# Kernel tuning notes

Measured on AMD Instinct MI355X. Metric: run time of the kernel, lower is better.

Reference implementation:

```python
import jax, jax.numpy as jnp
import numpy as np

B, C, H, W = 8, 384, 32, 32
NH = 6
HD = C // NH          # 64
T = H * W             # 1024
EPS = 1e-5            # torch InstanceNorm2d default


def setup_inputs() -> dict:
    key = jax.random.key(0)
    ks = jax.random.split(key, 8)
    s = 1.0 / np.sqrt(C)  # keep pre-softmax logits in a sane range
    x = jax.random.normal(ks[0], (B, C, H, W), dtype=jnp.float32)
    Wq = jax.random.normal(ks[1], (C, C), dtype=jnp.float32) * s
    Wk = jax.random.normal(ks[2], (C, C), dtype=jnp.float32) * s
    Wv = jax.random.normal(ks[3], (C, C), dtype=jnp.float32) * s
    head_w = jax.random.normal(ks[4], (NH, NH), dtype=jnp.float32) * (1.0 / np.sqrt(NH))
    gamma = jnp.ones((NH,), dtype=jnp.float32)
    beta = jnp.zeros((NH,), dtype=jnp.float32)
    projW = jax.random.normal(ks[5], (C, C), dtype=jnp.float32) * s
    projb = jnp.zeros((C,), dtype=jnp.float32)
    return {"x": x, "Wq": Wq, "Wk": Wk, "Wv": Wv, "head_w": head_w,
            "gamma": gamma, "beta": beta, "projW": projW, "projb": projb}


def reference(x, Wq, Wk, Wv, head_w, gamma, beta, projW, projb):
    b, c, h, w = x.shape
    t = h * w
    scale = HD ** (-0.5)
    xf = x.reshape(b, c, t)                               # [B,C,T]
    # 1x1 convs == channel GEMMs; conv weight [Cout,Cin]
    q = jnp.einsum('oc,bct->bot', Wq, xf).reshape(b, NH, HD, t)
    k = jnp.einsum('oc,bct->bot', Wk, xf).reshape(b, NH, HD, t)
    v = jnp.einsum('oc,bct->bot', Wv, xf).reshape(b, NH, HD, t)
    # raw scores [B,h,T,T], scaled
    scores = jnp.einsum('bhdq,bhdt->bhqt', q, k) * scale
    # cross-head 1x1 conv mix: out-head g from in-head h
    mixed = jnp.einsum('gh,bhqt->bgqt', head_w, scores)
    attn = jax.nn.softmax(mixed, axis=-1)
    # InstanceNorm2d over spatial dims (q,T) per (b,head), biased variance
    mean = jnp.mean(attn, axis=(2, 3), keepdims=True)
    var = jnp.var(attn, axis=(2, 3), keepdims=True)
    attn = (attn - mean) * jax.lax.rsqrt(var + EPS)
    attn = attn * gamma[None, :, None, None] + beta[None, :, None, None]
    # value matmul: v is [B,h,d,T]
    out = jnp.einsum('bhqt,bhdt->bhqd', attn, v)          # [B,h,T,d]
    # faithful row-major reshape (matches torch .view(B, T, C))
    out = out.reshape(b, t, c)
    y = out @ projW.T + projb                              # Linear(C,C)
    return jnp.transpose(y, (0, 2, 1)).reshape(b, c, h, w)
```

## Files before the change

kernel.cpp:

```cpp
#include <hip/hip_runtime.h>
#include <hip/hip_bf16.h>
#include <cstdint>

typedef __bf16 bf16_t;
typedef __bf16 bf16x8 __attribute__((ext_vector_type(8)));
typedef float  f32x4  __attribute__((ext_vector_type(4)));

#define MFMA16(a, b, c) __builtin_amdgcn_mfma_f32_16x16x32_bf16((a), (b), (c), 0, 0, 0)

constexpr int BB = 8, CC = 384, NHH = 6, TT = 1024;

union U8 { uint4 u; bf16_t h[8]; };
union U2 { unsigned int u; bf16_t h[2]; };

struct CastArgs {
    const void* src[9];
    bf16_t*     dst[9];
    int         n[9];
};

__global__ __launch_bounds__(256) void cast_kernel(CastArgs a)
{
    const bool isbf = (((const unsigned short*)a.src[5])[0] == 0x3F80u);
    const int ai = blockIdx.y;
    const int n  = a.n[ai];
    bf16_t* dst  = a.dst[ai];
    const int t0     = (blockIdx.x * 256 + threadIdx.x) * 8;
    const int stride = gridDim.x * 256 * 8;
    if (isbf) {
        const bf16_t* s = (const bf16_t*)a.src[ai];
        for (int idx = t0; idx < n; idx += stride) {
            if (idx + 8 <= n) *(uint4*)(dst + idx) = *(const uint4*)(s + idx);
            else for (int j = 0; idx + j < n; ++j) dst[idx + j] = s[idx + j];
        }
    } else {
        const float* s = (const float*)a.src[ai];
        for (int idx = t0; idx < n; idx += stride) {
            if (idx + 8 <= n) {
                f32x4 v0 = *(const f32x4*)(s + idx);
                f32x4 v1 = *(const f32x4*)(s + idx + 4);
                U8 o;
                #pragma unroll
                for (int j = 0; j < 4; ++j) { o.h[j] = (bf16_t)v0[j]; o.h[4 + j] = (bf16_t)v1[j]; }
                *(uint4*)(dst + idx) = o.u;
            } else for (int j = 0; idx + j < n; ++j) dst[idx + j] = (bf16_t)s[idx + j];
        }
    }
}

__global__ __launch_bounds__(256) void qkv_kernel(
    const bf16_t* __restrict__ x,
    const bf16_t* __restrict__ Wq,
    const bf16_t* __restrict__ Wk,
    const bf16_t* __restrict__ Wv,
    const bf16_t* __restrict__ head_w,
    bf16_t* __restrict__ Qmix,
    bf16_t* __restrict__ kT,
    bf16_t* __restrict__ vm)
{
    const int og = blockIdx.x;
    const int tt = blockIdx.y;
    const int b  = blockIdx.z;
    const int t0 = tt * 64;
    const int tid  = threadIdx.x;
    const int lane = tid & 63;
    const int wid  = tid >> 6;
    const int quad = lane >> 4;
    const int l16  = lane & 15;

    __shared__ __align__(16) bf16_t xT[64][CC + 8];
    __shared__ float smixL[36];

    if (tid < 36) smixL[tid] = 0.125f * (float)head_w[tid];
    {
        const bf16_t* xb = x + (size_t)b * CC * TT;
        const int tq = tid & 7;
        const int cp = tid >> 3;
        #pragma unroll
        for (int pass = 0; pass < 6; ++pass) {
            const int c = (pass * 32 + cp) * 2;
            U8 r0, r1;
            r0.u = *(const uint4*)(xb + (size_t)c * TT + t0 + tq * 8);
            r1.u = *(const uint4*)(xb + (size_t)(c + 1) * TT + t0 + tq * 8);
            #pragma unroll
            for (int j = 0; j < 8; ++j) {
                U2 p; p.h[0] = r0.h[j]; p.h[1] = r1.h[j];
                *(unsigned int*)&xT[tq * 8 + j][c] = p.u;
            }
        }
    }
    __syncthreads();

    const bf16_t* W = (og < 2) ? Wq : (og < 4) ? Wk : Wv;
    const int obase = (og & 1) * 192 + wid * 48;

    if (og < 4) {
        f32x4 acc[3][4];
        const f32x4 zero = {0.f, 0.f, 0.f, 0.f};
        #pragma unroll
        for (int mi = 0; mi < 3; ++mi)
            #pragma unroll
            for (int ni = 0; ni < 4; ++ni) acc[mi][ni] = zero;

        for (int k0 = 0; k0 < CC; k0 += 32) {
            bf16x8 afr[3];
            #pragma unroll
            for (int mi = 0; mi < 3; ++mi)
                afr[mi] = *(const bf16x8*)(W + (size_t)(obase + mi * 16 + l16) * CC + k0 + quad * 8);
            #pragma unroll
            for (int ni = 0; ni < 4; ++ni) {
                bf16x8 bfr = *(const bf16x8*)&xT[ni * 16 + l16][k0 + quad * 8];
                #pragma unroll
                for (int mi = 0; mi < 3; ++mi)
                    acc[mi][ni] = MFMA16(afr[mi], bfr, acc[mi][ni]);
            }
        }

        if (og < 2) {
            for (int g = 0; g < 6; ++g) {
                bf16_t* dst = Qmix + (size_t)(b * NHH + g) * TT * CC;
                #pragma unroll
                for (int mi = 0; mi < 3; ++mi)
                    #pragma unroll
                    for (int ni = 0; ni < 4; ++ni) {
                        const int o0 = obase + mi * 16 + quad * 4;
                        const int tl = t0 + ni * 16 + l16;
                        const float m = smixL[g * 6 + (o0 >> 6)];
                        U2 lo2, hi2;
                        lo2.h[0] = (bf16_t)(acc[mi][ni][0] * m); lo2.h[1] = (bf16_t)(acc[mi][ni][1] * m);
                        hi2.h[0] = (bf16_t)(acc[mi][ni][2] * m); hi2.h[1] = (bf16_t)(acc[mi][ni][3] * m);
                        uint2 pk; pk.x = lo2.u; pk.y = hi2.u;
                        *(uint2*)(dst + (size_t)tl * CC + o0) = pk;
                    }
            }
        } else {
            #pragma unroll
            for (int mi = 0; mi < 3; ++mi)
                #pragma unroll
                for (int ni = 0; ni < 4; ++ni) {
                    const int o0 = obase + mi * 16 + quad * 4;
                    const int tl = t0 + ni * 16 + l16;
                    U2 lo2, hi2;
                    lo2.h[0] = (bf16_t)acc[mi][ni][0]; lo2.h[1] = (bf16_t)acc[mi][ni][1];
                    hi2.h[0] = (bf16_t)acc[mi][ni][2]; hi2.h[1] = (bf16_t)acc[mi][ni][3];
                    uint2 pk; pk.x = lo2.u; pk.y = hi2.u;
                    *(uint2*)(kT + ((size_t)b * TT + tl) * CC + o0) = pk;
                }
        }
    } else {
        f32x4 acc[4][3];
        const f32x4 zero = {0.f, 0.f, 0.f, 0.f};
        #pragma unroll
        for (int mi = 0; mi < 4; ++mi)
            #pragma unroll
            for (int ni = 0; ni < 3; ++ni) acc[mi][ni] = zero;

        for (int k0 = 0; k0 < CC; k0 += 32) {
            bf16x8 bfr[3];
            #pragma unroll
            for (int ni = 0; ni < 3; ++ni)
                bfr[ni] = *(const bf16x8*)(W + (size_t)(obase + ni * 16 + l16) * CC + k0 + quad * 8);
            #pragma unroll
            for (int mi = 0; mi < 4; ++mi) {
                bf16x8 afr = *(const bf16x8*)&xT[mi * 16 + l16][k0 + quad * 8];
                #pragma unroll
                for (int ni = 0; ni < 3; ++ni)
                    acc[mi][ni] = MFMA16(afr, bfr[ni], acc[mi][ni]);
            }
        }

        #pragma unroll
        for (int mi = 0; mi < 4; ++mi)
            #pragma unroll
            for (int ni = 0; ni < 3; ++ni) {
                const int ol  = obase + ni * 16 + l16;
                const int tl0 = mi * 16 + quad * 4;
                U2 lo2, hi2;
                lo2.h[0] = (bf16_t)acc[mi][ni][0]; lo2.h[1] = (bf16_t)acc[mi][ni][1];
                hi2.h[0] = (bf16_t)acc[mi][ni][2]; hi2.h[1] = (bf16_t)acc[mi][ni][3];
                uint2 pk; pk.x = lo2.u; pk.y = hi2.u;
                *(uint2*)(vm + ((size_t)b * CC + ol) * TT + t0 + tl0) = pk;
            }
    }
}

__global__ __launch_bounds__(256) void vrow_kernel(const bf16_t* __restrict__ vm,
                                                   float* __restrict__ vrs)
{
    const int bg = blockIdx.x;
    const int d  = threadIdx.x & 63;
    const int qr = threadIdx.x >> 6;
    const bf16_t* row = vm + ((size_t)(bg / 6) * CC + (bg % 6) * 64 + d) * TT + qr * 256;
    float s = 0.f;
    for (int i = 0; i < 256; i += 8) {
        U8 v; v.u = *(const uint4*)(row + i);
        #pragma unroll
        for (int j = 0; j < 8; ++j) s += (float)v.h[j];
    }
    __shared__ float red[4][64];
    red[qr][d] = s;
    __syncthreads();
    if (qr == 0) vrs[bg * 64 + d] = red[0][d] + red[1][d] + red[2][d] + red[3][d];
}

__global__ __launch_bounds__(256, 3) void fused_attn(
    const bf16_t* __restrict__ Qmix,
    const bf16_t* __restrict__ kT,
    const bf16_t* __restrict__ vm,
    float* __restrict__ Uhat,
    float* __restrict__ sumsq)
{
    const int L  = blockIdx.x;
    const int b  = L & 7;
    const int rr = L >> 3;
    const int qt = rr & 15;
    const int g  = rr >> 4;
    const int qbase = qt * 64;
    const int tid = threadIdx.x, lane = tid & 63, wid = tid >> 6;
    const int quad = lane >> 4, l16 = lane & 15;
    const int Msub = (wid & 1) * 64;
    const int Nsub = (wid >> 1) * 32;

    __shared__ __align__(16) bf16_t sm[12288];
    bf16_t* At = sm;
    bf16_t* Bt = sm + 8192;
    bf16_t* Ps = sm;
    bf16_t* Vt = sm + 4096;
    __shared__ float lred[4][2][16], l2red[4][2][16];
    __shared__ float lrowS[64];

    const bf16_t* kTb = kT + (size_t)b * TT * CC;
    const bf16_t* Qb  = Qmix + ((size_t)(b * NHH + g) * TT + qbase) * CC;
    const bf16_t* Vb  = vm + ((size_t)b * CC + g * 64) * TT;

    float lacc[2] = {0.f, 0.f}, l2acc[2] = {0.f, 0.f};
    f32x4 U[4];
    const f32x4 zero = {0.f, 0.f, 0.f, 0.f};
    #pragma unroll
    for (int n2 = 0; n2 < 4; ++n2) U[n2] = zero;

    for (int tt = 0; tt < 8; ++tt) {
        f32x4 S[4][2];
        #pragma unroll
        for (int mi = 0; mi < 4; ++mi)
            #pragma unroll
            for (int ni = 0; ni < 2; ++ni) S[mi][ni] = zero;

        for (int kk = 0; kk < 6; ++kk) {
            __syncthreads();
            #pragma unroll
            for (int it = 0; it < 4; ++it) {
                const int id = it * 256 + tid;
                const int row = id >> 3, ch = id & 7;
                U8 v; v.u = *(const uint4*)(kTb + (size_t)(tt * 128 + row) * CC + kk * 64 + ch * 8);
                *(uint4*)&At[row * 64 + ((ch ^ (row & 7)) * 8)] = v.u;
            }
            #pragma unroll
            for (int it = 0; it < 2; ++it) {
                const int id = it * 256 + tid;
                const int row = id >> 3, ch = id & 7;
                U8 v; v.u = *(const uint4*)(Qb + (size_t)row * CC + kk * 64 + ch * 8);
                *(uint4*)&Bt[row * 64 + ((ch ^ (row & 7)) * 8)] = v.u;
            }
            __syncthreads();
            #pragma unroll
            for (int k2 = 0; k2 < 2; ++k2) {
                const int sw = ((k2 * 4 + quad) ^ (l16 & 7)) * 8;
                bf16x8 a[4], bq[2];
                #pragma unroll
                for (int mi = 0; mi < 4; ++mi)
                    a[mi] = *(const bf16x8*)&At[(Msub + mi * 16 + l16) * 64 + sw];
                #pragma unroll
                for (int ni = 0; ni < 2; ++ni)
                    bq[ni] = *(const bf16x8*)&Bt[(Nsub + ni * 16 + l16) * 64 + sw];
                #pragma unroll
                for (int mi = 0; mi < 4; ++mi)
                    #pragma unroll
                    for (int ni = 0; ni < 2; ++ni)
                        S[mi][ni] = MFMA16(a[mi], bq[ni], S[mi][ni]);
            }
        }

        #pragma unroll
        for (int mi = 0; mi < 4; ++mi)
            #pragma unroll
            for (int ni = 0; ni < 2; ++ni)
                #pragma unroll
                for (int r = 0; r < 4; ++r) {
                    const float p = __expf(fminf(S[mi][ni][r], 60.0f));
                    S[mi][ni][r] = p;
                    lacc[ni]  += p;
                    l2acc[ni] += p * p;
                }

        __syncthreads();

        #pragma unroll
        for (int it = 0; it < 4; ++it) {
            const int id = it * 256 + tid;
            const int row = id >> 4, ch = id & 15;
            U8 v; v.u = *(const uint4*)(Vb + (size_t)row * TT + tt * 128 + ch * 8);
            *(uint4*)&Vt[row * 128 + ((((ch & 7) ^ (row & 7)) | (ch & 8)) * 8)] = v.u;
        }

        #pragma unroll
        for (int h = 0; h < 2; ++h) {
            if ((wid & 1) == h) {
                #pragma unroll
                for (int mi = 0; mi < 4; ++mi) {
                    const int tc = mi * 2 + (quad >> 1);
                    #pragma unroll
                    for (int ni = 0; ni < 2; ++ni) {
                        const int q = Nsub + ni * 16 + l16;
                        U2 lo2, hi2;
                        lo2.h[0] = (bf16_t)S[mi][ni][0]; lo2.h[1] = (bf16_t)S[mi][ni][1];
                        hi2.h[0] = (bf16_t)S[mi][ni][2]; hi2.h[1] = (bf16_t)S[mi][ni][3];
                        uint2 pk; pk.x = lo2.u; pk.y = hi2.u;
                        *(uint2*)&Ps[q * 64 + ((tc ^ (l16 & 7)) * 8) + (quad & 1) * 4] = pk;
                    }
                }
            }
            __syncthreads();
            bf16x8 ap[2];
            #pragma unroll
            for (int k2 = 0; k2 < 2; ++k2) {
                const int qa = wid * 16 + l16;
                ap[k2] = *(const bf16x8*)&Ps[qa * 64 + (((k2 * 4 + quad) ^ (l16 & 7)) * 8)];
            }
            #pragma unroll
            for (int n2 = 0; n2 < 4; ++n2) {
                const int d = n2 * 16 + l16;
                #pragma unroll
                for (int k2 = 0; k2 < 2; ++k2) {
                    const int tc = h * 8 + k2 * 4 + quad;
                    bf16x8 bv = *(const bf16x8*)&Vt[d * 128 + ((((tc & 7) ^ (l16 & 7)) | (tc & 8)) * 8)];
                    U[n2] = MFMA16(ap[k2], bv, U[n2]);
                }
            }
            __syncthreads();
        }
    }

    #pragma unroll
    for (int ni = 0; ni < 2; ++ni) {
        float l = lacc[ni], l2 = l2acc[ni];
        l  += __shfl_xor(l, 16, 64);  l  += __shfl_xor(l, 32, 64);
        l2 += __shfl_xor(l2, 16, 64); l2 += __shfl_xor(l2, 32, 64);
        if (quad == 0) { lred[wid][ni][l16] = l; l2red[wid][ni][l16] = l2; }
    }
    __syncthreads();
    if (tid < 64) {
        const int q = tid;
        const int w0 = (q >> 5) * 2, ni = (q >> 4) & 1, lo = q & 15;
        const float l  = lred[w0][ni][lo]  + lred[w0 + 1][ni][lo];
        const float l2 = l2red[w0][ni][lo] + l2red[w0 + 1][ni][lo];
        lrowS[q] = l;
        float c = l2 / (l * l);
        #pragma unroll
        for (int off = 1; off < 64; off <<= 1) c += __shfl_xor(c, off, 64);
        if (tid == 0) atomicAdd(&sumsq[b * NHH + g], c);
    }
    __syncthreads();

    float* Ub = Uhat + ((size_t)(b * NHH + g) * TT + qbase) * 64;
    #pragma unroll
    for (int r = 0; r < 4; ++r) {
        const int ql = wid * 16 + quad * 4 + r;
        const float invl = 1.0f / lrowS[ql];
        #pragma unroll
        for (int n2 = 0; n2 < 4; ++n2)
            Ub[(size_t)ql * 64 + n2 * 16 + l16] = U[n2][r] * invl;
    }
}

__global__ __launch_bounds__(256) void proj_kernel(
    const float* __restrict__ Uhat,
    const float* __restrict__ vrs,
    const float* __restrict__ sumsq,
    const bf16_t* __restrict__ gamma,
    const bf16_t* __restrict__ beta,
    const bf16_t* __restrict__ projW,
    const bf16_t* __restrict__ projb,
    float* __restrict__ out)
{
    const int ts = blockIdx.x;
    const int b  = blockIdx.y;
    const int t0 = ts * 32;
    const int tid = threadIdx.x, lane = tid & 63, wid = tid >> 6;
    const int quad = lane >> 4, l16 = lane & 15;

    __shared__ float Ac[6], Cc[6], pb[CC];
    if (tid < 6) {
        const float ss  = sumsq[b * NHH + tid];
        const float var = fmaxf(ss - 1.0f, 0.0f) * (1.0f / 1048576.0f);
        const float a   = (float)gamma[tid] * rsqrtf(var + 1e-5f);
        Ac[tid] = a;
        Cc[tid] = (float)beta[tid] - a * (1.0f / 1024.0f);
    }
    for (int i = tid; i < CC; i += 256) pb[i] = (float)projb[i];
    __syncthreads();

    f32x4 acc[6][2];
    const f32x4 zero = {0.f, 0.f, 0.f, 0.f};
    #pragma unroll
    for (int mi = 0; mi < 6; ++mi)
        #pragma unroll
        for (int ni = 0; ni < 2; ++ni) acc[mi][ni] = zero;

    const float* Ub = Uhat + (size_t)b * TT * CC;
    for (int k0 = 0; k0 < CC; k0 += 32) {
        bf16x8 bfr[2];
        #pragma unroll
        for (int ni = 0; ni < 2; ++ni) {
            const int tl = t0 + ni * 16 + l16;
            const int baseoff = tl * CC + k0 + quad * 8;
            f32x4 u0 = *(const f32x4*)(Ub + baseoff);
            f32x4 u1 = *(const f32x4*)(Ub + baseoff + 4);
            U8 z;
            #pragma unroll
            for (int j = 0; j < 8; ++j) {
                const int off = baseoff + j;
                const int h = off >> 16;
                const int d = off & 63;
                const float uv = (j < 4) ? u0[j] : u1[j - 4];
                z.h[j] = (bf16_t)(Ac[h] * uv + Cc[h] * vrs[(b * NHH + h) * 64 + d]);
            }
            bfr[ni] = *(const bf16x8*)&z;
        }
        #pragma unroll
        for (int mi = 0; mi < 6; ++mi) {
            const int o = wid * 96 + mi * 16 + l16;
            bf16x8 afr = *(const bf16x8*)(projW + (size_t)o * CC + k0 + quad * 8);
            #pragma unroll
            for (int ni = 0; ni < 2; ++ni)
                acc[mi][ni] = MFMA16(afr, bfr[ni], acc[mi][ni]);
        }
    }

    #pragma unroll
    for (int mi = 0; mi < 6; ++mi)
        #pragma unroll
        for (int ni = 0; ni < 2; ++ni)
            #pragma unroll
            for (int r = 0; r < 4; ++r) {
                const int o  = wid * 96 + mi * 16 + quad * 4 + r;
                const int tl = t0 + ni * 16 + l16;
                out[((size_t)b * CC + o) * TT + tl] = acc[mi][ni][r] + pb[o];
            }
}

extern "C" void kernel_launch(void* const* d_in, const int* in_sizes, int n_in,
                              void* d_out, int out_size, void* d_ws, size_t ws_size,
                              hipStream_t stream)
{
    float* outp = (float*)d_out;
    char* ws = (char*)d_ws;

    size_t off = 0;
    auto alloc = [&](size_t bytes) {
        void* p = ws + off;
        off += (bytes + 255) & ~(size_t)255;
        return p;
    };

    const size_t szQ = (size_t)BB * TT * CC * sizeof(bf16_t);

    bf16_t* cx  = (bf16_t*)alloc(szQ);
    bf16_t* cWq = (bf16_t*)alloc((size_t)CC * CC * 2);
    bf16_t* cWk = (bf16_t*)alloc((size_t)CC * CC * 2);
    bf16_t* cWv = (bf16_t*)alloc((size_t)CC * CC * 2);
    bf16_t* cPW = (bf16_t*)alloc((size_t)CC * CC * 2);
    bf16_t* chw = (bf16_t*)alloc(64 * 2);
    bf16_t* cg  = (bf16_t*)alloc(64 * 2);
    bf16_t* cb  = (bf16_t*)alloc(64 * 2);
    bf16_t* cpb = (bf16_t*)alloc(CC * 2);
    bf16_t* Qm  = (bf16_t*)alloc((size_t)BB * NHH * TT * CC * 2);
    bf16_t* kT  = (bf16_t*)alloc(szQ);
    bf16_t* vm  = (bf16_t*)alloc(szQ);
    float*  Uh  = (float*)alloc((size_t)BB * NHH * TT * 64 * 4);
    float*  vr  = (float*)alloc(48 * 64 * 4);
    float*  sq  = (float*)alloc(48 * 4);

    CastArgs ca;
    bf16_t* dsts[9] = {cx, cWq, cWk, cWv, chw, cg, cb, cPW, cpb};
    for (int i = 0; i < 9; ++i) {
        ca.src[i] = d_in[i];
        ca.dst[i] = dsts[i];
        ca.n[i]   = in_sizes[i];
    }

    hipMemsetAsync(sq, 0, 48 * sizeof(float), stream);
    cast_kernel<<<dim3(192, 9), 256, 0, stream>>>(ca);
    qkv_kernel<<<dim3(6, 16, 8), 256, 0, stream>>>(cx, cWq, cWk, cWv, chw, Qm, kT, vm);
    vrow_kernel<<<48, 256, 0, stream>>>(vm, vr);
    fused_attn<<<768, 256, 0, stream>>>(Qm, kT, vm, Uh, sq);
    proj_kernel<<<dim3(32, 8), 256, 0, stream>>>(Uh, vr, sq, cg, cb, cPW, cpb, outp);
}
```

Measured before the change: 219.0 us.

## Apply head mixing on score tiles in-kernel instead of materializing per-head mixed Q

Stops writing six head-mixed copies of Q. The attention kernel now computes raw per-head scores for all six heads at once, mixes them across heads in registers, and then takes the exponential. It splits the key range into two halves across blocks, with double-buffered K/V loads staged through registers. It also adds a stats kernel that merges the partial row sums and square sums and moves the 1/l normalization into the projection. This removes a large Q write and read and the repeated K reads per mixed head, at the cost of more registers, 512-thread blocks, and partial U buffers that the projection must sum.

```diff
diff --git a/kernel.cpp b/kernel.cpp
--- a/kernel.cpp
+++ b/kernel.cpp
@@ -53,8 +53,7 @@
     const bf16_t* __restrict__ Wq,
     const bf16_t* __restrict__ Wk,
     const bf16_t* __restrict__ Wv,
-    const bf16_t* __restrict__ head_w,
-    bf16_t* __restrict__ Qmix,
+    bf16_t* __restrict__ qT,
     bf16_t* __restrict__ kT,
     bf16_t* __restrict__ vm)
 {
@@ -69,9 +68,7 @@
     const int l16  = lane & 15;
 
     __shared__ __align__(16) bf16_t xT[64][CC + 8];
-    __shared__ float smixL[36];
-
-    if (tid < 36) smixL[tid] = 0.125f * (float)head_w[tid];
+
     {
         const bf16_t* xb = x + (size_t)b * CC * TT;
         const int tq = tid & 7;
@@ -116,37 +113,19 @@
             }
         }
 
-        if (og < 2) {
-            for (int g = 0; g < 6; ++g) {
-                bf16_t* dst = Qmix + (size_t)(b * NHH + g) * TT * CC;
-                #pragma unroll
-                for (int mi = 0; mi < 3; ++mi)
-                    #pragma unroll
-                    for (int ni = 0; ni < 4; ++ni) {
-                        const int o0 = obase + mi * 16 + quad * 4;
-                        const int tl = t0 + ni * 16 + l16;
-                        const float m = smixL[g * 6 + (o0 >> 6)];
-                        U2 lo2, hi2;
-                        lo2.h[0] = (bf16_t)(acc[mi][ni][0] * m); lo2.h[1] = (bf16_t)(acc[mi][ni][1] * m);
-                        hi2.h[0] = (bf16_t)(acc[mi][ni][2] * m); hi2.h[1] = (bf16_t)(acc[mi][ni][3] * m);
-                        uint2 pk; pk.x = lo2.u; pk.y = hi2.u;
-                        *(uint2*)(dst + (size_t)tl * CC + o0) = pk;
-                    }
-            }
-        } else {
-            #pragma unroll
-            for (int mi = 0; mi < 3; ++mi)
-                #pragma unroll
-                for (int ni = 0; ni < 4; ++ni) {
-                    const int o0 = obase + mi * 16 + quad * 4;
-                    const int tl = t0 + ni * 16 + l16;
-                    U2 lo2, hi2;
-                    lo2.h[0] = (bf16_t)acc[mi][ni][0]; lo2.h[1] = (bf16_t)acc[mi][ni][1];
-                    hi2.h[0] = (bf16_t)acc[mi][ni][2]; hi2.h[1] = (bf16_t)acc[mi][ni][3];
-                    uint2 pk; pk.x = lo2.u; pk.y = hi2.u;
-                    *(uint2*)(kT + ((size_t)b * TT + tl) * CC + o0) = pk;
-                }
-        }
+        bf16_t* dst = (og < 2) ? qT : kT;
+        #pragma unroll
+        for (int mi = 0; mi < 3; ++mi)
+            #pragma unroll
+            for (int ni = 0; ni < 4; ++ni) {
+                const int o0 = obase + mi * 16 + quad * 4;
+                const int tl = t0 + ni * 16 + l16;
+                U2 lo2, hi2;
+                lo2.h[0] = (bf16_t)acc[mi][ni][0]; lo2.h[1] = (bf16_t)acc[mi][ni][1];
+                hi2.h[0] = (bf16_t)acc[mi][ni][2]; hi2.h[1] = (bf16_t)acc[mi][ni][3];
+                uint2 pk; pk.x = lo2.u; pk.y = hi2.u;
+                *(uint2*)(dst + ((size_t)b * TT + tl) * CC + o0) = pk;
+            }
     } else {
         f32x4 acc[4][3];
         const f32x4 zero = {0.f, 0.f, 0.f, 0.f};
@@ -203,178 +182,219 @@
     if (qr == 0) vrs[bg * 64 + d] = red[0][d] + red[1][d] + red[2][d] + red[3][d];
 }
 
-__global__ __launch_bounds__(256, 3) void fused_attn(
-    const bf16_t* __restrict__ Qmix,
+__global__ __launch_bounds__(512, 2) void fused_attn(
+    const bf16_t* __restrict__ qT,
     const bf16_t* __restrict__ kT,
     const bf16_t* __restrict__ vm,
-    float* __restrict__ Uhat,
-    float* __restrict__ sumsq)
+    const bf16_t* __restrict__ head_w,
+    float* __restrict__ Up,
+    float* __restrict__ lp,
+    float* __restrict__ l2p)
 {
     const int L  = blockIdx.x;
     const int b  = L & 7;
     const int rr = L >> 3;
     const int qt = rr & 15;
-    const int g  = rr >> 4;
-    const int qbase = qt * 64;
+    const int th = rr >> 4;
+
     const int tid = threadIdx.x, lane = tid & 63, wid = tid >> 6;
     const int quad = lane >> 4, l16 = lane & 15;
-    const int Msub = (wid & 1) * 64;
-    const int Nsub = (wid >> 1) * 32;
-
-    __shared__ __align__(16) bf16_t sm[12288];
-    bf16_t* At = sm;
-    bf16_t* Bt = sm + 8192;
-    bf16_t* Ps = sm;
-    bf16_t* Vt = sm + 4096;
-    __shared__ float lred[4][2][16], l2red[4][2][16];
-    __shared__ float lrowS[64];
-
-    const bf16_t* kTb = kT + (size_t)b * TT * CC;
-    const bf16_t* Qb  = Qmix + ((size_t)(b * NHH + g) * TT + qbase) * CC;
-    const bf16_t* Vb  = vm + ((size_t)b * CC + g * 64) * TT;
-
-    float lacc[2] = {0.f, 0.f}, l2acc[2] = {0.f, 0.f};
-    f32x4 U[4];
+
+    __shared__ __align__(16) bf16_t sm[49152];
+    bf16_t* Ks = sm;
+    bf16_t* Ps = sm + 12288;
+    bf16_t* Vs = sm + 24576;
+    __shared__ float smix[36];
+
+    if (tid < 36) smix[tid] = 0.125f * (float)head_w[tid];
+
+    const int T0 = th * 512;
+
+    const int tsub = wid & 1;
+    const int sqh  = wid >> 1;
+    const int pqg  = wid >> 1;
+    const int pgg  = wid & 1;
+
+    bf16x8 qf[6][2];
+    {
+        const bf16_t* Qb = qT + ((size_t)b * TT + qt * 64 + sqh * 16 + l16) * CC + quad * 8;
+        #pragma unroll
+        for (int kk = 0; kk < 6; ++kk)
+            #pragma unroll
+            for (int k2 = 0; k2 < 2; ++k2)
+                qf[kk][k2] = *(const bf16x8*)(Qb + kk * 64 + k2 * 32);
+    }
+
+    const bf16_t* ksrc[3]; const bf16_t* vsrc[3];
+    int kdst[3], vdst[3];
+    #pragma unroll
+    for (int it = 0; it < 3; ++it) {
+        const int f  = it * 512 + tid;
+        const int kk = f >> 8, krow = (f >> 3) & 31, kch = f & 7;
+        ksrc[it] = kT + ((size_t)b * TT + T0 + krow) * CC + kk * 64 + (kch ^ (krow & 7)) * 8;
+        kdst[it] = f * 8;
+        const int vrow = f >> 2, vch = f & 3;
+        vsrc[it] = vm + ((size_t)b * CC + vrow) * TT + T0 + (vch ^ ((vrow >> 1) & 3)) * 8;
+        vdst[it] = f * 8;
+    }
+
+    uint4 kreg[3], vreg[3];
+    #pragma unroll
+    for (int it = 0; it < 3; ++it) {
+        kreg[it] = *(const uint4*)ksrc[it];
+        vreg[it] = *(const uint4*)vsrc[it];
+    }
+    __syncthreads();
+
+    float mixc[36];
+    #pragma unroll
+    for (int j = 0; j < 36; ++j)
+        mixc[j] = __uint_as_float(__builtin_amdgcn_readfirstlane(__float_as_uint(smix[j])));
+
+    #pragma unroll
+    for (int it = 0; it < 3; ++it) {
+        *(uint4*)&Ks[kdst[it]] = kreg[it];
+        *(uint4*)&Vs[vdst[it]] = vreg[it];
+        kreg[it] = *(const uint4*)(ksrc[it] + 32 * CC);
+        vreg[it] = *(const uint4*)(vsrc[it] + 32);
+    }
+    __syncthreads();
+
+    f32x4 Uacc[3][4];
     const f32x4 zero = {0.f, 0.f, 0.f, 0.f};
     #pragma unroll
-    for (int n2 = 0; n2 < 4; ++n2) U[n2] = zero;
-
-    for (int tt = 0; tt < 8; ++tt) {
-        f32x4 S[4][2];
-        #pragma unroll
-        for (int mi = 0; mi < 4; ++mi)
-            #pragma unroll
-            for (int ni = 0; ni < 2; ++ni) S[mi][ni] = zero;
-
+    for (int hh = 0; hh < 3; ++hh)
+        #pragma unroll
+        for (int n2 = 0; n2 < 4; ++n2) Uacc[hh][n2] = zero;
+    float lacc[6]  = {0.f, 0.f, 0.f, 0.f, 0.f, 0.f};
+    float l2acc[6] = {0.f, 0.f, 0.f, 0.f, 0.f, 0.f};
+
+    const int arow  = (tsub * 16 + l16) * 64;
+    const int aswz0 = ((quad)     ^ (l16 & 7)) * 8;
+    const int aswz1 = ((4 + quad) ^ (l16 & 7)) * 8;
+    const int prow  = (sqh * 16 + l16) * 32;
+    const int pswzW = ((tsub * 2 + (quad >> 1)) ^ ((l16 >> 1) & 3)) * 8 + (quad & 1) * 4;
+    const int parow = (pqg * 16 + l16) * 32;
+    const int pswzR = (quad ^ ((l16 >> 1) & 3)) * 8;
+
+    for (int t = 0; t < 16; ++t) {
+        f32x4 S[6];
+        #pragma unroll
         for (int kk = 0; kk < 6; ++kk) {
-            __syncthreads();
-            #pragma unroll
-            for (int it = 0; it < 4; ++it) {
-                const int id = it * 256 + tid;
-                const int row = id >> 3, ch = id & 7;
-                U8 v; v.u = *(const uint4*)(kTb + (size_t)(tt * 128 + row) * CC + kk * 64 + ch * 8);
-                *(uint4*)&At[row * 64 + ((ch ^ (row & 7)) * 8)] = v.u;
-            }
-            #pragma unroll
-            for (int it = 0; it < 2; ++it) {
-                const int id = it * 256 + tid;
-                const int row = id >> 3, ch = id & 7;
-                U8 v; v.u = *(const uint4*)(Qb + (size_t)row * CC + kk * 64 + ch * 8);
-                *(uint4*)&Bt[row * 64 + ((ch ^ (row & 7)) * 8)] = v.u;
-            }
-            __syncthreads();
-            #pragma unroll
-            for (int k2 = 0; k2 < 2; ++k2) {
-                const int sw = ((k2 * 4 + quad) ^ (l16 & 7)) * 8;
-                bf16x8 a[4], bq[2];
+            bf16x8 a0 = *(const bf16x8*)&Ks[kk * 2048 + arow + aswz0];
+            bf16x8 a1 = *(const bf16x8*)&Ks[kk * 2048 + arow + aswz1];
+            S[kk] = MFMA16(a0, qf[kk][0], zero);
+            S[kk] = MFMA16(a1, qf[kk][1], S[kk]);
+        }
+        uint2 pk[6];
+        #pragma unroll
+        for (int g = 0; g < 6; ++g) {
+            float mp[4];
+            #pragma unroll
+            for (int r = 0; r < 4; ++r) {
+                float m = mixc[g * 6] * S[0][r];
                 #pragma unroll
-                for (int mi = 0; mi < 4; ++mi)
-                    a[mi] = *(const bf16x8*)&At[(Msub + mi * 16 + l16) * 64 + sw];
-                #pragma unroll
-                for (int ni = 0; ni < 2; ++ni)
-                    bq[ni] = *(const bf16x8*)&Bt[(Nsub + ni * 16 + l16) * 64 + sw];
-                #pragma unroll
-                for (int mi = 0; mi < 4; ++mi)
-                    #pragma unroll
-                    for (int ni = 0; ni < 2; ++ni)
-                        S[mi][ni] = MFMA16(a[mi], bq[ni], S[mi][ni]);
-            }
-        }
-
-        #pragma unroll
-        for (int mi = 0; mi < 4; ++mi)
-            #pragma unroll
-            for (int ni = 0; ni < 2; ++ni)
-                #pragma unroll
-                for (int r = 0; r < 4; ++r) {
-                    const float p = __expf(fminf(S[mi][ni][r], 60.0f));
-                    S[mi][ni][r] = p;
-                    lacc[ni]  += p;
-                    l2acc[ni] += p * p;
-                }
-
+                for (int h = 1; h < 6; ++h) m += mixc[g * 6 + h] * S[h][r];
+                const float p = __expf(fminf(m, 60.0f));
+                lacc[g]  += p;
+                l2acc[g] += p * p;
+                mp[r] = p;
+            }
+            U2 lo, hi;
+            lo.h[0] = (bf16_t)mp[0]; lo.h[1] = (bf16_t)mp[1];
+            hi.h[0] = (bf16_t)mp[2]; hi.h[1] = (bf16_t)mp[3];
+            pk[g].x = lo.u; pk[g].y = hi.u;
+        }
         __syncthreads();
-
-        #pragma unroll
-        for (int it = 0; it < 4; ++it) {
-            const int id = it * 256 + tid;
-            const int row = id >> 4, ch = id & 15;
-            U8 v; v.u = *(const uint4*)(Vb + (size_t)row * TT + tt * 128 + ch * 8);
-            *(uint4*)&Vt[row * 128 + ((((ch & 7) ^ (row & 7)) | (ch & 8)) * 8)] = v.u;
-        }
-
-        #pragma unroll
-        for (int h = 0; h < 2; ++h) {
-            if ((wid & 1) == h) {
-                #pragma unroll
-                for (int mi = 0; mi < 4; ++mi) {
-                    const int tc = mi * 2 + (quad >> 1);
-                    #pragma unroll
-                    for (int ni = 0; ni < 2; ++ni) {
-                        const int q = Nsub + ni * 16 + l16;
-                        U2 lo2, hi2;
-                        lo2.h[0] = (bf16_t)S[mi][ni][0]; lo2.h[1] = (bf16_t)S[mi][ni][1];
-                        hi2.h[0] = (bf16_t)S[mi][ni][2]; hi2.h[1] = (bf16_t)S[mi][ni][3];
-                        uint2 pk; pk.x = lo2.u; pk.y = hi2.u;
-                        *(uint2*)&Ps[q * 64 + ((tc ^ (l16 & 7)) * 8) + (quad & 1) * 4] = pk;
-                    }
-                }
-            }
-            __syncthreads();
-            bf16x8 ap[2];
-            #pragma unroll
-            for (int k2 = 0; k2 < 2; ++k2) {
-                const int qa = wid * 16 + l16;
-                ap[k2] = *(const bf16x8*)&Ps[qa * 64 + (((k2 * 4 + quad) ^ (l16 & 7)) * 8)];
-            }
+        #pragma unroll
+        for (int it = 0; it < 3; ++it) {
+            *(uint4*)&Ks[kdst[it]] = kreg[it];
+            *(uint4*)&Vs[((t + 1) & 1) * 12288 + vdst[it]] = vreg[it];
+        }
+        #pragma unroll
+        for (int g = 0; g < 6; ++g)
+            *(uint2*)&Ps[g * 2048 + prow + pswzW] = pk[g];
+        {
+            const int nt = ((t + 2) & 15) * 32;
+            #pragma unroll
+            for (int it = 0; it < 3; ++it) {
+                kreg[it] = *(const uint4*)(ksrc[it] + nt * CC);
+                vreg[it] = *(const uint4*)(vsrc[it] + nt);
+            }
+        }
+        __syncthreads();
+        const int vb = (t & 1) * 12288;
+        #pragma unroll
+        for (int hh = 0; hh < 3; ++hh) {
+            const int g = pgg * 3 + hh;
+            bf16x8 ap = *(const bf16x8*)&Ps[g * 2048 + parow + pswzR];
             #pragma unroll
             for (int n2 = 0; n2 < 4; ++n2) {
-                const int d = n2 * 16 + l16;
-                #pragma unroll
-                for (int k2 = 0; k2 < 2; ++k2) {
-                    const int tc = h * 8 + k2 * 4 + quad;
-                    bf16x8 bv = *(const bf16x8*)&Vt[d * 128 + ((((tc & 7) ^ (l16 & 7)) | (tc & 8)) * 8)];
-                    U[n2] = MFMA16(ap[k2], bv, U[n2]);
-                }
-            }
-            __syncthreads();
-        }
-    }
-
-    #pragma unroll
-    for (int ni = 0; ni < 2; ++ni) {
-        float l = lacc[ni], l2 = l2acc[ni];
+                bf16x8 bv = *(const bf16x8*)&Vs[vb + (g * 64 + n2 * 16 + l16) * 32 + pswzR];
+                Uacc[hh][n2] = MFMA16(ap, bv, Uacc[hh][n2]);
+            }
+        }
+        __syncthreads();
+    }
+
+    float* lredL  = (float*)sm;
+    float* l2redL = lredL + 768;
+    #pragma unroll
+    for (int g = 0; g < 6; ++g) {
+        float l = lacc[g], l2 = l2acc[g];
         l  += __shfl_xor(l, 16, 64);  l  += __shfl_xor(l, 32, 64);
         l2 += __shfl_xor(l2, 16, 64); l2 += __shfl_xor(l2, 32, 64);
-        if (quad == 0) { lred[wid][ni][l16] = l; l2red[wid][ni][l16] = l2; }
-    }
-    __syncthreads();
-    if (tid < 64) {
-        const int q = tid;
-        const int w0 = (q >> 5) * 2, ni = (q >> 4) & 1, lo = q & 15;
-        const float l  = lred[w0][ni][lo]  + lred[w0 + 1][ni][lo];
-        const float l2 = l2red[w0][ni][lo] + l2red[w0 + 1][ni][lo];
-        lrowS[q] = l;
-        float c = l2 / (l * l);
-        #pragma unroll
-        for (int off = 1; off < 64; off <<= 1) c += __shfl_xor(c, off, 64);
-        if (tid == 0) atomicAdd(&sumsq[b * NHH + g], c);
-    }
-    __syncthreads();
-
-    float* Ub = Uhat + ((size_t)(b * NHH + g) * TT + qbase) * 64;
-    #pragma unroll
-    for (int r = 0; r < 4; ++r) {
-        const int ql = wid * 16 + quad * 4 + r;
-        const float invl = 1.0f / lrowS[ql];
+        if (quad == 0) {
+            lredL [wid * 96 + g * 16 + l16] = l;
+            l2redL[wid * 96 + g * 16 + l16] = l2;
+        }
+    }
+    __syncthreads();
+    if (tid < 384) {
+        const int g = tid >> 6, q = tid & 63;
+        const int w0 = (q >> 4) * 2, lo = q & 15;
+        const float l  = lredL [w0 * 96 + g * 16 + lo] + lredL [(w0 + 1) * 96 + g * 16 + lo];
+        const float l2 = l2redL[w0 * 96 + g * 16 + lo] + l2redL[(w0 + 1) * 96 + g * 16 + lo];
+        const size_t o = ((size_t)th * 48 + b * 6 + g) * TT + qt * 64 + q;
+        lp[o] = l; l2p[o] = l2;
+    }
+
+    #pragma unroll
+    for (int hh = 0; hh < 3; ++hh) {
+        const int g = pgg * 3 + hh;
+        float* Ub = Up + ((((size_t)th * 8 + b) * 6 + g) * TT + qt * 64 + pqg * 16) * 64;
         #pragma unroll
         for (int n2 = 0; n2 < 4; ++n2)
-            Ub[(size_t)ql * 64 + n2 * 16 + l16] = U[n2][r] * invl;
-    }
+            #pragma unroll
+            for (int r = 0; r < 4; ++r)
+                Ub[(size_t)(quad * 4 + r) * 64 + n2 * 16 + l16] = Uacc[hh][n2][r];
+    }
+}
+
+__global__ __launch_bounds__(256) void stats_kernel(
+    const float* __restrict__ lp, const float* __restrict__ l2p,
+    float* __restrict__ linv, float* __restrict__ sq)
+{
+    const int bg = blockIdx.x, tid = threadIdx.x;
+    float c = 0.f;
+    for (int q = tid; q < TT; q += 256) {
+        const float l  = lp [(size_t)bg * TT + q] + lp [(size_t)(48 + bg) * TT + q];
+        const float l2 = l2p[(size_t)bg * TT + q] + l2p[(size_t)(48 + bg) * TT + q];
+        const float inv = 1.0f / l;
+        linv[bg * TT + q] = inv;
+        c += l2 * inv * inv;
+    }
+    #pragma unroll
+    for (int off = 1; off < 64; off <<= 1) c += __shfl_xor(c, off, 64);
+    __shared__ float red[4];
+    if ((tid & 63) == 0) red[tid >> 6] = c;
+    __syncthreads();
+    if (tid == 0) sq[bg] = red[0] + red[1] + red[2] + red[3];
 }
 
 __global__ __launch_bounds__(256) void proj_kernel(
-    const float* __restrict__ Uhat,
+    const float* __restrict__ Up,
+    const float* __restrict__ linv,
     const float* __restrict__ vrs,
     const float* __restrict__ sumsq,
     const bf16_t* __restrict__ gamma,
@@ -407,23 +427,28 @@
         #pragma unroll
         for (int ni = 0; ni < 2; ++ni) acc[mi][ni] = zero;
 
-    const float* Ub = Uhat + (size_t)b * TT * CC;
+    const float* U0 = Up + (size_t)b * (NHH * TT * 64);
+    const float* U1 = Up + (size_t)(8 + b) * (NHH * TT * 64);
     for (int k0 = 0; k0 < CC; k0 += 32) {
         bf16x8 bfr[2];
         #pragma unroll
         for (int ni = 0; ni < 2; ++ni) {
             const int tl = t0 + ni * 16 + l16;
             const int baseoff = tl * CC + k0 + quad * 8;
-            f32x4 u0 = *(const f32x4*)(Ub + baseoff);
-            f32x4 u1 = *(const f32x4*)(Ub + baseoff + 4);
+            const int hh = baseoff >> 16;
+            const float li = linv[b * 6144 + (baseoff >> 6)];
+            const float A  = Ac[hh];
+            const float Cb = Cc[hh];
+            f32x4 a0 = *(const f32x4*)(U0 + baseoff);
+            f32x4 a1 = *(const f32x4*)(U0 + baseoff + 4);
+            f32x4 c0 = *(const f32x4*)(U1 + baseoff);
+            f32x4 c1 = *(const f32x4*)(U1 + baseoff + 4);
             U8 z;
             #pragma unroll
             for (int j = 0; j < 8; ++j) {
-                const int off = baseoff + j;
-                const int h = off >> 16;
-                const int d = off & 63;
-                const float uv = (j < 4) ? u0[j] : u1[j - 4];
-                z.h[j] = (bf16_t)(Ac[h] * uv + Cc[h] * vrs[(b * NHH + h) * 64 + d]);
+                const int d = (baseoff + j) & 63;
+                const float uv = ((j < 4) ? (a0[j] + c0[j]) : (a1[j - 4] + c1[j - 4])) * li;
+                z.h[j] = (bf16_t)(A * uv + Cb * vrs[(b * NHH + hh) * 64 + d]);
             }
             bfr[ni] = *(const bf16x8*)&z;
         }
@@ -463,9 +488,9 @@
         return p;
     };
 
-    const size_t szQ = (size_t)BB * TT * CC * sizeof(bf16_t);
-
-    bf16_t* cx  = (bf16_t*)alloc(szQ);
+    const size_t szT = (size_t)BB * TT * CC * sizeof(bf16_t);
+
+    bf16_t* cx  = (bf16_t*)alloc(szT);
     bf16_t* cWq = (bf16_t*)alloc((size_t)CC * CC * 2);
     bf16_t* cWk = (bf16_t*)alloc((size_t)CC * CC * 2);
     bf16_t* cWv = (bf16_t*)alloc((size_t)CC * CC * 2);
@@ -474,12 +499,15 @@
     bf16_t* cg  = (bf16_t*)alloc(64 * 2);
     bf16_t* cb  = (bf16_t*)alloc(64 * 2);
     bf16_t* cpb = (bf16_t*)alloc(CC * 2);
-    bf16_t* Qm  = (bf16_t*)alloc((size_t)BB * NHH * TT * CC * 2);
-    bf16_t* kT  = (bf16_t*)alloc(szQ);
-    bf16_t* vm  = (bf16_t*)alloc(szQ);
-    float*  Uh  = (float*)alloc((size_t)BB * NHH * TT * 64 * 4);
-    float*  vr  = (float*)alloc(48 * 64 * 4);
-    float*  sq  = (float*)alloc(48 * 4);
+    bf16_t* qTb = (bf16_t*)alloc(szT);
+    bf16_t* kTb = (bf16_t*)alloc(szT);
+    bf16_t* vmb = (bf16_t*)alloc(szT);
+    float*  Uh  = (float*)alloc((size_t)2 * BB * NHH * TT * 64 * sizeof(float));
+    float*  lpb = (float*)alloc((size_t)2 * 48 * TT * sizeof(float));
+    float*  l2b = (float*)alloc((size_t)2 * 48 * TT * sizeof(float));
+    float*  lv  = (float*)alloc((size_t)48 * TT * sizeof(float));
+    float*  vr  = (float*)alloc(48 * 64 * sizeof(float));
+    float*  sq  = (float*)alloc(48 * sizeof(float));
 
     CastArgs ca;
     bf16_t* dsts[9] = {cx, cWq, cWk, cWv, chw, cg, cb, cPW, cpb};
@@ -489,10 +517,10 @@
         ca.n[i]   = in_sizes[i];
     }
 
-    hipMemsetAsync(sq, 0, 48 * sizeof(float), stream);
     cast_kernel<<<dim3(192, 9), 256, 0, stream>>>(ca);
-    qkv_kernel<<<dim3(6, 16, 8), 256, 0, stream>>>(cx, cWq, cWk, cWv, chw, Qm, kT, vm);
-    vrow_kernel<<<48, 256, 0, stream>>>(vm, vr);
-    fused_attn<<<768, 256, 0, stream>>>(Qm, kT, vm, Uh, sq);
-    proj_kernel<<<dim3(32, 8), 256, 0, stream>>>(Uh, vr, sq, cg, cb, cPW, cpb, outp);
-}
+    qkv_kernel<<<dim3(6, 16, 8), 256, 0, stream>>>(cx, cWq, cWk, cWv, qTb, kTb, vmb);
+    vrow_kernel<<<48, 256, 0, stream>>>(vmb, vr);
+    fused_attn<<<256, 512, 0, stream>>>(qTb, kTb, vmb, chw, Uh, lpb, l2b);
+    stats_kernel<<<48, 256, 0, stream>>>(lpb, l2b, lv, sq);
+    proj_kernel<<<dim3(32, 8), 256, 0, stream>>>(Uh, lv, vr, sq, cg, cb, cPW, cpb, outp);
+}
```

Measured after the change: 223.7 us. 2.1% more time.
